# Kernel tuning notes

Measured on AMD Instinct MI355X. Metric: run time of the kernel, lower is better.

Reference implementation:

```python
import jax, jax.numpy as jnp
import numpy as np

N_USERS = 100000
N_ITEMS = 50000
DIM = 64
HID = 64
E = 3200000
B = 16384


def setup_inputs() -> dict:
    key = jax.random.key(0)
    ks = jax.random.split(key, 16)
    N = N_USERS + N_ITEMS
    return {
        "users": jax.random.randint(ks[0], (B,), 0, N_USERS),
        "items": jax.random.randint(ks[1], (B,), 0, N_ITEMS),
        "edge_index": jax.random.randint(ks[2], (2, E), 0, N),
        "edge_weight": jax.random.uniform(ks[3], (E,), dtype=jnp.float32),
        # learned parameters
        "U": jax.random.normal(ks[4], (N_USERS, DIM), jnp.float32) * 0.1,
        "I": jax.random.normal(ks[5], (N_ITEMS, DIM), jnp.float32) * 0.1,
        "W0": jax.random.normal(ks[6], (DIM, HID), jnp.float32) / np.sqrt(DIM),
        "b0": jnp.zeros((HID,), jnp.float32),
        "g0": jnp.ones((HID,), jnp.float32),
        "be0": jnp.zeros((HID,), jnp.float32),
        "W1": jax.random.normal(ks[7], (HID, HID), jnp.float32) / np.sqrt(HID),
        "b1": jnp.zeros((HID,), jnp.float32),
        "g1": jnp.ones((HID,), jnp.float32),
        "be1": jnp.zeros((HID,), jnp.float32),
        "Wp": jax.random.normal(ks[8], (HID, DIM), jnp.float32) / np.sqrt(HID),
        "bp": jnp.zeros((DIM,), jnp.float32),
        "bu": jnp.zeros((N_USERS,), jnp.float32),
        "bi": jnp.zeros((N_ITEMS,), jnp.float32),
        "mu": jnp.zeros((), jnp.float32),
    }


def _layernorm(h, g, b, eps=1e-5):
    m = jnp.mean(h, axis=-1, keepdims=True)
    v = jnp.mean(jnp.square(h - m), axis=-1, keepdims=True)
    return (h - m) * jax.lax.rsqrt(v + eps) * g + b


def reference(users, items, edge_index, edge_weight, U, I,
              W0, b0, g0, be0, W1, b1, g1, be1, Wp, bp, bu, bi, mu):
    N = U.shape[0] + I.shape[0]
    x = jnp.concatenate([U, I], axis=0)  # [N, DIM]

    # GCN normalization with added self-loops (torch_geometric gcn_norm)
    loop = jnp.arange(N)
    src = jnp.concatenate([edge_index[0], loop])
    dst = jnp.concatenate([edge_index[1], loop])
    ew = jnp.concatenate([edge_weight, jnp.ones((N,), edge_weight.dtype)])
    deg = jax.ops.segment_sum(ew, dst, num_segments=N)
    dinv = jnp.where(deg > 0, jax.lax.rsqrt(deg), 0.0)
    norm = dinv[src] * ew * dinv[dst]  # [E+N]

    def conv(h, W, b):
        hw = h @ W  # [N, HID]
        msgs = norm[:, None] * hw[src]  # gather: [E+N, HID]
        return jax.ops.segment_sum(msgs, dst, num_segments=N) + b

    # layer 0: conv -> layernorm -> relu -> (dropout=identity, eval) -> residual
    h = x
    h_in = h
    h = conv(h, W0, b0)
    h = jax.nn.relu(_layernorm(h, g0, be0)) + h_in
    # layer 1
    h_in = h
    h = conv(h, W1, b1)
    h = jax.nn.relu(_layernorm(h, g1, be1)) + h_in

    h = h @ Wp + bp  # proj_out: [N, DIM]
    h_user = h[:U.shape[0]]
    h_item = h[U.shape[0]:]

    s = jnp.sum(h_user[users] * h_item[items], axis=-1)
    s = s + bu[users] + bi[items] + mu
    return jnp.clip(s, 1.0, 5.0)
```

## Files before the change

kernel.cpp:

```cpp
#include <hip/hip_runtime.h>

#define NU 100000
#define NI 50000
#define NN 150000
#define D  64
#define CAP 47
#define OVF_MAX 4096

#define BINSHIFT 8
#define BINW 256
#define NBINS 586
#define BINCAP 5848
#define STAGE_CAP 11
#define EPT 8
#define BIN_BLOCKS 768
#define BCPAD 16
#define TAILS 5

typedef unsigned int uint;
typedef unsigned short ushort;
typedef unsigned char uchar;

__device__ __forceinline__ float half_reduce_add(float v) {
    #pragma unroll
    for (int m = 16; m >= 1; m >>= 1) v += __shfl_xor(v, m, 64);
    return v;
}
__device__ __forceinline__ ushort f2bf(float f) {
    union { float f; uint i; } c; c.f = f;
    uint r = c.i + 0x7FFF + ((c.i >> 16) & 1);
    return (ushort)(r >> 16);
}
__device__ __forceinline__ float lane_bcast(float v, int l) {
    return __int_as_float(__builtin_amdgcn_readlane(__float_as_int(v), l));
}
__device__ __forceinline__ uint enc14(float w) {
    uint b = __float_as_uint(w) + 0x00020000u;
    return b & 0xFFFC0000u;
}
__device__ __forceinline__ float dec14(uint r) {
    return __uint_as_float(r & 0xFFFC0000u);
}

__global__ __launch_bounds__(256) void k_bin(
        const int* __restrict__ src, const int* __restrict__ dst,
        const float* __restrict__ ew, int* __restrict__ bincur,
        uint2* __restrict__ binbuf, uint2* __restrict__ tail,
        uchar* __restrict__ cnt8, int E) {
    __shared__ uint2 stage[NBINS][STAGE_CAP];
    __shared__ int scnt[NBINS];
    int t = threadIdx.x;
    for (int i = t; i < NBINS; i += 256) scnt[i] = 0;
    __syncthreads();
    const int batch = 256 * EPT;
    for (int base = blockIdx.x * batch; base < E; base += BIN_BLOCKS * batch) {
        int dd[EPT]; uint ss[EPT]; float ww[EPT]; int ok[EPT];
        #pragma unroll
        for (int k = 0; k < EPT; ++k) {
            int e = base + k * 256 + t;
            ok[k] = (e < E);
            if (ok[k]) { dd[k] = dst[e]; ss[k] = (uint)src[e]; ww[k] = ew[e]; }
        }
        #pragma unroll
        for (int k = 0; k < EPT; ++k) {
            if (!ok[k]) continue;
            int bin = dd[k] >> BINSHIFT;
            uint2 rec = make_uint2(
                ss[k] | ((uint)(dd[k] & (BINW - 1)) << 18),
                (uint)__float_as_int(ww[k]));
            int slot = atomicAdd(&scnt[bin], 1);
            if (slot < STAGE_CAP) {
                stage[bin][slot] = rec;
            } else {
                int b0 = atomicAdd(&bincur[bin * BCPAD], 1);
                if (b0 < BINCAP) binbuf[(size_t)bin * BINCAP + b0] = rec;
            }
        }
        __syncthreads();
        for (int bin = t; bin < NBINS; bin += 256) {
            int c = scnt[bin]; if (c > STAGE_CAP) c = STAGE_CAP;
            while (c >= 8) {
                int b0 = atomicAdd(&bincur[bin * BCPAD], 8);
                if (b0 + 8 <= BINCAP) {
                    uint4* o4 = (uint4*)(binbuf + (size_t)bin * BINCAP + b0);
                    uint2* s2 = &stage[bin][c - 8];
                    o4[0] = make_uint4(s2[0].x, s2[0].y, s2[1].x, s2[1].y);
                    o4[1] = make_uint4(s2[2].x, s2[2].y, s2[3].x, s2[3].y);
                    o4[2] = make_uint4(s2[4].x, s2[4].y, s2[5].x, s2[5].y);
                    o4[3] = make_uint4(s2[6].x, s2[6].y, s2[7].x, s2[7].y);
                }
                c -= 8;
            }
            scnt[bin] = c;
        }
        __syncthreads();
    }
    uchar* cb = cnt8 + (size_t)blockIdx.x * NBINS;
    for (int bin = t; bin < NBINS; bin += 256) {
        int c = scnt[bin]; if (c > STAGE_CAP) c = STAGE_CAP;
        if (c > TAILS) {
            for (int j = TAILS; j < c; ++j) {
                int b0 = atomicAdd(&bincur[bin * BCPAD], 1);
                if (b0 < BINCAP) binbuf[(size_t)bin * BINCAP + b0] =
                    stage[bin][j];
            }
            c = TAILS;
        }
        cb[bin] = (uchar)c;
    }
    uint2* tb = tail + (size_t)blockIdx.x * (NBINS * TAILS);
    for (int i = t; i < NBINS * TAILS; i += 256)
        tb[i] = stage[i / TAILS][i % TAILS];
}

__global__ __launch_bounds__(256) void k_regroup(
        const int* __restrict__ bincur, const uint2* __restrict__ binbuf,
        const uint2* __restrict__ tail, const uchar* __restrict__ cnt8,
        uint* __restrict__ recs, int* __restrict__ cursor,
        float* __restrict__ dinv, int4* __restrict__ ovf,
        int* __restrict__ ovfcnt,
        const float* __restrict__ U, const float* __restrict__ I,
        const float* __restrict__ W0, ushort* __restrict__ hw2b) {
    __shared__ uint image[256 * CAP];
    __shared__ int cnt[256];
    __shared__ float ovfw[256];
    int t = threadIdx.x;
    int bin = blockIdx.x;
    cnt[t] = 0; ovfw[t] = 0.0f;
    __syncthreads();
    int dbase = bin << BINSHIFT;
    int nrec = bincur[bin * BCPAD]; if (nrec > BINCAP) nrec = BINCAP;
    const uint2* bb = binbuf + (size_t)bin * BINCAP;
    for (int i = t; i < nrec; i += 256) {
        uint2 r = bb[i];
        int dl = (int)(r.x >> 18);
        int slot = atomicAdd(&cnt[dl], 1);
        uint s = r.x & 0x3FFFFu;
        float w = __int_as_float((int)r.y);
        if (slot < CAP) image[dl * CAP + slot] = enc14(w) | s;
        else {
            atomicAdd(&ovfw[dl], w);
            int o = atomicAdd(ovfcnt, 1);
            if (o < OVF_MAX)
                ovf[o] = make_int4(dbase + dl, (int)s, __float_as_int(w), 0);
        }
    }
    for (int g = t; g < BIN_BLOCKS; g += 256) {
        int c = cnt8[(size_t)g * NBINS + bin];
        const uint2* tb = tail + ((size_t)g * NBINS + bin) * TAILS;
        for (int j = 0; j < c; ++j) {
            uint2 r = tb[j];
            int dl = (int)(r.x >> 18);
            int slot = atomicAdd(&cnt[dl], 1);
            uint s = r.x & 0x3FFFFu;
            float w = __int_as_float((int)r.y);
            if (slot < CAP) image[dl * CAP + slot] = enc14(w) | s;
            else {
                atomicAdd(&ovfw[dl], w);
                int o = atomicAdd(ovfcnt, 1);
                if (o < OVF_MAX)
                    ovf[o] = make_int4(dbase + dl, (int)s, __float_as_int(w), 0);
            }
        }
    }
    __syncthreads();
    int ndl = NN - dbase; if (ndl > 256) ndl = 256;
    if (ndl <= 0) return;
    if (t < ndl) {
        int c = cnt[t];
        cursor[dbase + t] = c;
        if (c > CAP) c = CAP;
        float dg = ovfw[t];
        for (int j = 0; j < c; ++j) dg += dec14(image[t * CAP + j]);
        float dv = rsqrtf(dg + 1.0f);
        dinv[dbase + t] = dv;
        ovfw[t] = dv;
    }
    int tot = ndl * CAP;
    uint* out = recs + (size_t)dbase * CAP;
    for (int i = t; i < tot; i += 256) out[i] = image[i];
    __syncthreads();
    {
        int lane = t & 63;
        int wv = t >> 6;
        float wreg[64];
        #pragma unroll
        for (int k = 0; k < 64; ++k) wreg[k] = W0[k * 64 + lane];
        for (int j = wv; j < ndl; j += 4) {
            int n = dbase + j;
            float xv = (n < NU) ? U[(size_t)n * D + lane]
                                : I[(size_t)(n - NU) * D + lane];
            float a0 = 0.f, a1 = 0.f, a2 = 0.f, a3 = 0.f;
            #pragma unroll
            for (int k = 0; k < 64; k += 4) {
                a0 = fmaf(lane_bcast(xv, k + 0), wreg[k + 0], a0);
                a1 = fmaf(lane_bcast(xv, k + 1), wreg[k + 1], a1);
                a2 = fmaf(lane_bcast(xv, k + 2), wreg[k + 2], a2);
                a3 = fmaf(lane_bcast(xv, k + 3), wreg[k + 3], a3);
            }
            hw2b[(size_t)n * D + lane] =
                f2bf(((a0 + a1) + (a2 + a3)) * ovfw[j]);
        }
    }
}

#define CA_DECL(c) uint x##c##0, x##c##1, x##c##2, x##c##3, \
                        w##c##0, w##c##1, w##c##2, w##c##3;
#define CA_GET(c, i, P, rvv) { \
    uint r = (uint)__builtin_amdgcn_ds_bpermute(vodd4 + 8 * (P), (int)(rvv)); \
    w##c##i = r & 0xFFFC0000u; \
    x##c##i = *(const uint*)((const char*)hw2p + \
                             (((r & 0x3FFFFu) << 7) + lb4)); }
#define CA_ISSUE(c, P0, rvv) { CA_GET(c, 0, (P0)+0, rvv) CA_GET(c, 1, (P0)+1, rvv) \
                               CA_GET(c, 2, (P0)+2, rvv) CA_GET(c, 3, (P0)+3, rvv) }
#define CA_FMA1(c, i, axv, ayv) { \
    axv = fmaf(__uint_as_float(w##c##i), __uint_as_float(x##c##i << 16), axv); \
    ayv = fmaf(__uint_as_float(w##c##i), \
               __uint_as_float(x##c##i & 0xFFFF0000u), ayv); }
#define CA_FMA(c, axv, ayv) { CA_FMA1(c,0,axv,ayv) CA_FMA1(c,1,axv,ayv) \
                              CA_FMA1(c,2,axv,ayv) CA_FMA1(c,3,axv,ayv) }

__device__ __forceinline__ float2 conv_accum2(int n, int lane,
        const uint* __restrict__ hw2p, const int* __restrict__ cursor,
        const uint* __restrict__ recs, const int4* __restrict__ ovf,
        const int* __restrict__ ovfcnt) {
    int cnt = __builtin_amdgcn_readfirstlane(cursor[n]);
    if (cnt > CAP) cnt = CAP;
    uint rv = (lane < cnt) ? recs[(size_t)n * CAP + lane] : 0u;
    const int  vodd4 = (lane >> 5) << 2;
    const uint lb4   = (uint)(lane & 31) << 2;
    uint xs = *(const uint*)((const char*)hw2p + (((uint)n << 7) + lb4));
    float ax = 0.f, ay = 0.f;
    int cp = (cnt + 7) & ~7;
    CA_DECL(A) CA_DECL(B) CA_DECL(G)
    CA_ISSUE(A, 0, rv) CA_ISSUE(B, 4, rv) CA_ISSUE(G, 8, rv)
    CA_FMA(A, ax, ay)
    if (cp > 24) CA_ISSUE(A, 12, rv)
    CA_FMA(B, ax, ay)
    if (cp > 32) CA_ISSUE(B, 16, rv)
    CA_FMA(G, ax, ay)
    if (cp > 40) CA_ISSUE(G, 20, rv)
    if (cp > 24) CA_FMA(A, ax, ay)
    if (cp > 32) CA_FMA(B, ax, ay)
    if (cp > 40) CA_FMA(G, ax, ay)
    ax += __shfl_xor(ax, 32, 64);
    ay += __shfl_xor(ay, 32, 64);
    ax += __uint_as_float(xs << 16);
    ay += __uint_as_float(xs & 0xFFFF0000u);
    int novf = __builtin_amdgcn_readfirstlane(ovfcnt[0]);
    if (novf > 0) {
        if (novf > OVF_MAX) novf = OVF_MAX;
        for (int j = 0; j < novf; ++j) {
            int4 e = ovf[j];
            if (e.x == n) {
                float w = __int_as_float(e.z);
                uint x = hw2p[(size_t)e.y * 32 + (lane & 31)];
                ax = fmaf(w, __int_as_float((int)(x << 16)), ax);
                ay = fmaf(w, __int_as_float((int)(x & 0xFFFF0000u)), ay);
            }
        }
    }
    return make_float2(ax, ay);
}

__device__ __forceinline__ float2 ln_relu2(float2 a, float di, int p,
        const float* __restrict__ b, const float* __restrict__ g,
        const float* __restrict__ be) {
    float2 bb = ((const float2*)b)[p];
    float v0 = fmaf(a.x, di, bb.x);
    float v1 = fmaf(a.y, di, bb.y);
    float m = half_reduce_add(v0 + v1) * (1.0f / 64.0f);
    float d0 = v0 - m, d1 = v1 - m;
    float var = half_reduce_add(d0 * d0 + d1 * d1) * (1.0f / 64.0f);
    float rs = rsqrtf(var + 1e-5f);
    float2 gg = ((const float2*)g)[p];
    float2 ee = ((const float2*)be)[p];
    return make_float2(fmaxf(fmaf(d0 * rs, gg.x, ee.x), 0.0f),
                       fmaxf(fmaf(d1 * rs, gg.y, ee.y), 0.0f));
}

__global__ __launch_bounds__(256) void k_conv1(
        const uint* __restrict__ hw2p, const int* __restrict__ cursor,
        const uint* __restrict__ recs, const int4* __restrict__ ovf,
        const int* __restrict__ ovfcnt, const float* __restrict__ dinv,
        const float* __restrict__ b, const float* __restrict__ g,
        const float* __restrict__ be, const float* __restrict__ U,
        const float* __restrict__ I, uint* __restrict__ out1) {
    int lane = threadIdx.x & 63;
    int n = __builtin_amdgcn_readfirstlane(blockIdx.x * 4 + (threadIdx.x >> 6));
    if (n >= NN) return;
    float2 a = conv_accum2(n, lane, hw2p, cursor, recs, ovf, ovfcnt);
    int p = lane & 31;
    float2 y = ln_relu2(a, dinv[n], p, b, g, be);
    const float* R = (n < NU) ? (U + (size_t)n * D) : (I + (size_t)(n - NU) * D);
    float2 rr = ((const float2*)R)[p];
    if (lane < 32) {
        out1[(size_t)n * 32 + p] =
            (uint)f2bf(y.x + rr.x) | ((uint)f2bf(y.y + rr.y) << 16);
    }
}

#define CB_DECL(p, c) uint p##x##c##0, p##x##c##1, p##x##c##2, p##x##c##3, \
                           p##w##c##0, p##w##c##1, p##w##c##2, p##w##c##3;
#define CB_GET(p, c, i, P, rvv) { \
    uint r = (uint)__builtin_amdgcn_ds_bpermute(vodd4 + 8 * (P), (int)(rvv)); \
    p##w##c##i = r & 0xFFFC0000u; \
    p##x##c##i = *(const uint*)((const char*)hw2p + \
                                (((r & 0x3FFFFu) << 7) + lb4)); }
#define CB_ISSUE(p, c, P0, rvv) { CB_GET(p,c,0,(P0)+0,rvv) CB_GET(p,c,1,(P0)+1,rvv) \
                                  CB_GET(p,c,2,(P0)+2,rvv) CB_GET(p,c,3,(P0)+3,rvv) }
#define CB_FMA1(p, c, i, axv, ayv) { \
    axv = fmaf(__uint_as_float(p##w##c##i), \
               __uint_as_float(p##x##c##i << 16), axv); \
    ayv = fmaf(__uint_as_float(p##w##c##i), \
               __uint_as_float(p##x##c##i & 0xFFFF0000u), ayv); }
#define CB_FMA(p, c, axv, ayv) { CB_FMA1(p,c,0,axv,ayv) CB_FMA1(p,c,1,axv,ayv) \
                                 CB_FMA1(p,c,2,axv,ayv) CB_FMA1(p,c,3,axv,ayv) }

__device__ __forceinline__ void conv_accum2_dual(int nu, int ni, int lane,
        const uint* __restrict__ hw2p, const int* __restrict__ cursor,
        const uint* __restrict__ recs, const int4* __restrict__ ovf,
        const int* __restrict__ ovfcnt, float2* outu, float2* outi) {
    int cu = __builtin_amdgcn_readfirstlane(cursor[nu]); if (cu > CAP) cu = CAP;
    int ci = __builtin_amdgcn_readfirstlane(cursor[ni]); if (ci > CAP) ci = CAP;
    uint rvu = (lane < cu) ? recs[(size_t)nu * CAP + lane] : 0u;
    uint rvi = (lane < ci) ? recs[(size_t)ni * CAP + lane] : 0u;
    const int  vodd4 = (lane >> 5) << 2;
    const uint lb4   = (uint)(lane & 31) << 2;
    uint xsu = *(const uint*)((const char*)hw2p + (((uint)nu << 7) + lb4));
    uint xsi = *(const uint*)((const char*)hw2p + (((uint)ni << 7) + lb4));
    float uax = 0.f, uay = 0.f, iax = 0.f, iay = 0.f;
    int cpu_ = (cu + 7) & ~7, cpi_ = (ci + 7) & ~7;
    CB_DECL(u, A) CB_DECL(u, B) CB_DECL(u, G)
    CB_DECL(i, A) CB_DECL(i, B) CB_DECL(i, G)
    CB_ISSUE(u, A, 0, rvu) CB_ISSUE(i, A, 0, rvi)
    CB_ISSUE(u, B, 4, rvu) CB_ISSUE(i, B, 4, rvi)
    CB_ISSUE(u, G, 8, rvu) CB_ISSUE(i, G, 8, rvi)
    CB_FMA(u, A, uax, uay) CB_FMA(i, A, iax, iay)
    if (cpu_ > 24) CB_ISSUE(u, A, 12, rvu)
    if (cpi_ > 24) CB_ISSUE(i, A, 12, rvi)
    CB_FMA(u, B, uax, uay) CB_FMA(i, B, iax, iay)
    if (cpu_ > 32) CB_ISSUE(u, B, 16, rvu)
    if (cpi_ > 32) CB_ISSUE(i, B, 16, rvi)
    CB_FMA(u, G, uax, uay) CB_FMA(i, G, iax, iay)
    if (cpu_ > 40) CB_ISSUE(u, G, 20, rvu)
    if (cpi_ > 40) CB_ISSUE(i, G, 20, rvi)
    if (cpu_ > 24) CB_FMA(u, A, uax, uay)
    if (cpi_ > 24) CB_FMA(i, A, iax, iay)
    if (cpu_ > 32) CB_FMA(u, B, uax, uay)
    if (cpi_ > 32) CB_FMA(i, B, iax, iay)
    if (cpu_ > 40) CB_FMA(u, G, uax, uay)
    if (cpi_ > 40) CB_FMA(i, G, iax, iay)
    uax += __shfl_xor(uax, 32, 64); uay += __shfl_xor(uay, 32, 64);
    iax += __shfl_xor(iax, 32, 64); iay += __shfl_xor(iay, 32, 64);
    uax += __uint_as_float(xsu << 16); uay += __uint_as_float(xsu & 0xFFFF0000u);
    iax += __uint_as_float(xsi << 16); iay += __uint_as_float(xsi & 0xFFFF0000u);
    int novf = __builtin_amdgcn_readfirstlane(ovfcnt[0]);
    if (novf > 0) {
        if (novf > OVF_MAX) novf = OVF_MAX;
        for (int j = 0; j < novf; ++j) {
            int4 e = ovf[j];
            if (e.x == nu || e.x == ni) {
                float w = __int_as_float(e.z);
                uint x = hw2p[(size_t)e.y * 32 + (lane & 31)];
                float fx = __uint_as_float(x << 16);
                float fy = __uint_as_float(x & 0xFFFF0000u);
                if (e.x == nu) { uax = fmaf(w, fx, uax); uay = fmaf(w, fy, uay); }
                else           { iax = fmaf(w, fx, iax); iay = fmaf(w, fy, iay); }
            }
        }
    }
    *outu = make_float2(uax, uay);
    *outi = make_float2(iax, iay);
}

__global__ __launch_bounds__(256) void k_gemm2(
        const ushort* __restrict__ hb, const float* __restrict__ W,
        const float* __restrict__ dinv, ushort* __restrict__ out) {
    int lane = threadIdx.x & 63;
    float wreg[64];
    #pragma unroll
    for (int k = 0; k < 64; ++k) wreg[k] = W[k * 64 + lane];
    int wpb = blockDim.x >> 6;
    int wid = blockIdx.x * wpb + (threadIdx.x >> 6);
    int tw = gridDim.x * wpb;
    for (int n = wid; n < NN; n += tw) {
        float xv = __uint_as_float((uint)hb[(size_t)n * D + lane] << 16);
        float a0 = 0.f, a1 = 0.f, a2 = 0.f, a3 = 0.f;
        #pragma unroll
        for (int k = 0; k < 64; k += 4) {
            a0 = fmaf(lane_bcast(xv, k + 0), wreg[k + 0], a0);
            a1 = fmaf(lane_bcast(xv, k + 1), wreg[k + 1], a1);
            a2 = fmaf(lane_bcast(xv, k + 2), wreg[k + 2], a2);
            a3 = fmaf(lane_bcast(xv, k + 3), wreg[k + 3], a3);
        }
        out[(size_t)n * D + lane] = f2bf(((a0 + a1) + (a2 + a3)) * dinv[n]);
    }
}

__global__ __launch_bounds__(256) void k_conv2score(
        const uint* __restrict__ hw2p, const int* __restrict__ cursor,
        const uint* __restrict__ recs, const int4* __restrict__ ovf,
        const int* __restrict__ ovfcnt, const float* __restrict__ dinv,
        const float* __restrict__ b, const float* __restrict__ g,
        const float* __restrict__ be, const int* __restrict__ users,
        const int* __restrict__ items, const uint* __restrict__ h1b,
        const float* __restrict__ Wp, const float* __restrict__ bp,
        const float* __restrict__ bu, const float* __restrict__ bi,
        const float* __restrict__ mu, float* __restrict__ out, int B) {
    __shared__ float wlds[64 * 64];
    int t = threadIdx.x;
    for (int i = t; i < 64 * 64; i += 256) wlds[i] = Wp[i];
    __syncthreads();
    int lane = t & 63;
    float bpl = bp[lane];
    int q = lane & 31;
    int wpb = blockDim.x >> 6;
    int wid = blockIdx.x * wpb + (t >> 6);
    int tw = gridDim.x * wpb;
    for (int p = wid; p < B; p += tw) {
        int un = users[p];
        int in_ = NU + items[p];
        int nu = __builtin_amdgcn_readfirstlane(un);
        int ni = __builtin_amdgcn_readfirstlane(in_);
        float2 au, ai;
        conv_accum2_dual(nu, ni, lane, hw2p, cursor, recs, ovf, ovfcnt,
                         &au, &ai);
        float2 yu = ln_relu2(au, dinv[nu], q, b, g, be);
        float2 yi = ln_relu2(ai, dinv[ni], q, b, g, be);
        uint xu = h1b[(size_t)nu * 32 + q];
        uint xi = h1b[(size_t)ni * 32 + q];
        float2 hu = make_float2(yu.x + __uint_as_float(xu << 16),
                                yu.y + __uint_as_float(xu & 0xFFFF0000u));
        float2 hi = make_float2(yi.x + __uint_as_float(xi << 16),
                                yi.y + __uint_as_float(xi & 0xFFFF0000u));
        float pu = bpl, pi = bpl;
        #pragma unroll
        for (int j = 0; j < 32; ++j) {
            float w0 = wlds[(2 * j) * 64 + lane];
            float w1 = wlds[(2 * j + 1) * 64 + lane];
            pu = fmaf(lane_bcast(hu.x, j), w0, pu);
            pu = fmaf(lane_bcast(hu.y, j), w1, pu);
            pi = fmaf(lane_bcast(hi.x, j), w0, pi);
            pi = fmaf(lane_bcast(hi.y, j), w1, pi);
        }
        float dot = pu * pi;
        #pragma unroll
        for (int m = 32; m >= 1; m >>= 1) dot += __shfl_xor(dot, m, 64);
        if (lane == 0) {
            dot += bu[un] + bi[in_ - NU] + mu[0];
            out[p] = fminf(fmaxf(dot, 1.0f), 5.0f);
        }
    }
}

extern "C" void kernel_launch(void* const* d_in, const int* in_sizes, int n_in,
                              void* d_out, int out_size, void* d_ws, size_t ws_size,
                              hipStream_t stream) {
    const int*   users = (const int*)d_in[0];
    const int*   items = (const int*)d_in[1];
    const int*   ei2   = (const int*)d_in[2];
    const float* ew    = (const float*)d_in[3];
    const float* U     = (const float*)d_in[4];
    const float* I     = (const float*)d_in[5];
    const float* W0    = (const float*)d_in[6];
    const float* b0    = (const float*)d_in[7];
    const float* g0    = (const float*)d_in[8];
    const float* be0   = (const float*)d_in[9];
    const float* W1    = (const float*)d_in[10];
    const float* b1    = (const float*)d_in[11];
    const float* g1    = (const float*)d_in[12];
    const float* be1   = (const float*)d_in[13];
    const float* Wp    = (const float*)d_in[14];
    const float* bp    = (const float*)d_in[15];
    const float* bu    = (const float*)d_in[16];
    const float* bi    = (const float*)d_in[17];
    const float* mu    = (const float*)d_in[18];

    int B = in_sizes[0];
    int E = in_sizes[2] / 2;
    const int* srcp = ei2;
    const int* dstp = ei2 + E;

    char* p = (char*)d_ws;
    auto alloc = [&](size_t bytes) -> char* {
        char* r = p;
        p += (bytes + 255) & ~(size_t)255;
        return r;
    };
    int*    cbuf    = (int*)  alloc((size_t)(NBINS * BCPAD + 32) * 4);
    int*    bincur  = cbuf;
    int*    ovfcnt  = cbuf + NBINS * BCPAD + 16;
    int*    cursor  = (int*)  alloc((size_t)NN * 4);
    float*  dinv    = (float*)alloc((size_t)NN * 4);
    int4*   ovf     = (int4*) alloc((size_t)OVF_MAX * 16);
    uchar*  cnt8    = (uchar*)alloc((size_t)BIN_BLOCKS * NBINS);
    uint2*  binbuf  = (uint2*)alloc((size_t)NBINS * BINCAP * 8);
    uint*   recs    = (uint*) alloc((size_t)NN * CAP * 4);
    ushort* hw2b    = (ushort*)alloc((size_t)NN * D * 2);
    uint*   h1b     = (uint*) alloc((size_t)NN * 32 * 4);
    const uint* hw2p = (const uint*)hw2b;
    uint2*  tail    = (uint2*)h1b;

    hipMemsetAsync(cbuf, 0, (size_t)(NBINS * BCPAD + 32) * 4, stream);

    int gW = (NN + 3) / 4;

    k_bin<<<BIN_BLOCKS, 256, 0, stream>>>(srcp, dstp, ew, bincur, binbuf,
                                          tail, cnt8, E);
    k_regroup<<<NBINS, 256, 0, stream>>>(bincur, binbuf, tail, cnt8,
                                         recs, cursor, dinv, ovf, ovfcnt,
                                         U, I, W0, hw2b);

    k_conv1<<<gW, 256, 0, stream>>>(hw2p, cursor, recs, ovf, ovfcnt, dinv,
                                    b0, g0, be0, U, I, h1b);
    k_gemm2<<<2048, 256, 0, stream>>>((const ushort*)h1b, W1, dinv, hw2b);
    k_conv2score<<<2048, 256, 0, stream>>>(hw2p, cursor, recs, ovf, ovfcnt, dinv,
                                           b1, g1, be1, users, items, h1b,
                                           Wp, bp, bu, bi, mu,
                                           (float*)d_out, B);
}
```

Before: 403.2 us.

## Transpose tail buffer to bin-major, embed counts in records, widen regroup blocks

The per-block tail records are now stored bin-major, so each regroup block reads a contiguous region instead of striding across blocks. The tail count is packed into the top bits of the first record, which removes the separate cnt8 array and its scattered byte reads. k_regroup runs with 512 threads to raise parallelism in the record scatter, the output copy and the W0 projection. Packing the count into bits 26+ assumes the destination-local field fits in 8 bits, which is why it is now masked; the W0 stage keeps 64 register floats per thread at double the block size, which may cost occupancy.

```diff
diff --git a/kernel.cpp b/kernel.cpp
--- a/kernel.cpp
+++ b/kernel.cpp
@@ -45,8 +45,7 @@
 __global__ __launch_bounds__(256) void k_bin(
         const int* __restrict__ src, const int* __restrict__ dst,
         const float* __restrict__ ew, int* __restrict__ bincur,
-        uint2* __restrict__ binbuf, uint2* __restrict__ tail,
-        uchar* __restrict__ cnt8, int E) {
+        uint2* __restrict__ binbuf, uint2* __restrict__ tail, int E) {
     __shared__ uint2 stage[NBINS][STAGE_CAP];
     __shared__ int scnt[NBINS];
     int t = threadIdx.x;
@@ -95,7 +94,6 @@
         }
         __syncthreads();
     }
-    uchar* cb = cnt8 + (size_t)blockIdx.x * NBINS;
     for (int bin = t; bin < NBINS; bin += 256) {
         int c = scnt[bin]; if (c > STAGE_CAP) c = STAGE_CAP;
         if (c > TAILS) {
@@ -106,16 +104,20 @@
             }
             c = TAILS;
         }
-        cb[bin] = (uchar)c;
-    }
-    uint2* tb = tail + (size_t)blockIdx.x * (NBINS * TAILS);
-    for (int i = t; i < NBINS * TAILS; i += 256)
-        tb[i] = stage[i / TAILS][i % TAILS];
-}
-
-__global__ __launch_bounds__(256) void k_regroup(
+        scnt[bin] = c;
+    }
+    __syncthreads();
+    for (int i = t; i < NBINS * TAILS; i += 256) {
+        int bin = i / TAILS, slot = i % TAILS;
+        uint2 r = stage[bin][slot];
+        if (slot == 0) r.x = (r.x & 0x03FFFFFFu) | ((uint)scnt[bin] << 26);
+        tail[((size_t)bin * BIN_BLOCKS + blockIdx.x) * TAILS + slot] = r;
+    }
+}
+
+__global__ __launch_bounds__(512) void k_regroup(
         const int* __restrict__ bincur, const uint2* __restrict__ binbuf,
-        const uint2* __restrict__ tail, const uchar* __restrict__ cnt8,
+        const uint2* __restrict__ tail,
         uint* __restrict__ recs, int* __restrict__ cursor,
         float* __restrict__ dinv, int4* __restrict__ ovf,
         int* __restrict__ ovfcnt,
@@ -126,12 +128,12 @@
     __shared__ float ovfw[256];
     int t = threadIdx.x;
     int bin = blockIdx.x;
-    cnt[t] = 0; ovfw[t] = 0.0f;
+    if (t < 256) { cnt[t] = 0; ovfw[t] = 0.0f; }
     __syncthreads();
     int dbase = bin << BINSHIFT;
     int nrec = bincur[bin * BCPAD]; if (nrec > BINCAP) nrec = BINCAP;
     const uint2* bb = binbuf + (size_t)bin * BINCAP;
-    for (int i = t; i < nrec; i += 256) {
+    for (int i = t; i < nrec; i += 512) {
         uint2 r = bb[i];
         int dl = (int)(r.x >> 18);
         int slot = atomicAdd(&cnt[dl], 1);
@@ -145,12 +147,15 @@
                 ovf[o] = make_int4(dbase + dl, (int)s, __float_as_int(w), 0);
         }
     }
-    for (int g = t; g < BIN_BLOCKS; g += 256) {
-        int c = cnt8[(size_t)g * NBINS + bin];
-        const uint2* tb = tail + ((size_t)g * NBINS + bin) * TAILS;
+    const uint2* tbin = tail + (size_t)bin * BIN_BLOCKS * TAILS;
+    for (int g = t; g < BIN_BLOCKS; g += 512) {
+        const uint2* tb = tbin + (size_t)g * TAILS;
+        uint2 r0 = tb[0];
+        int c = (int)(r0.x >> 26);
+        r0.x &= 0x03FFFFFFu;
         for (int j = 0; j < c; ++j) {
-            uint2 r = tb[j];
-            int dl = (int)(r.x >> 18);
+            uint2 r = (j == 0) ? r0 : tb[j];
+            int dl = (int)((r.x >> 18) & 0xFFu);
             int slot = atomicAdd(&cnt[dl], 1);
             uint s = r.x & 0x3FFFFu;
             float w = __int_as_float((int)r.y);
@@ -178,7 +183,7 @@
     }
     int tot = ndl * CAP;
     uint* out = recs + (size_t)dbase * CAP;
-    for (int i = t; i < tot; i += 256) out[i] = image[i];
+    for (int i = t; i < tot; i += 512) out[i] = image[i];
     __syncthreads();
     {
         int lane = t & 63;
@@ -186,7 +191,7 @@
         float wreg[64];
         #pragma unroll
         for (int k = 0; k < 64; ++k) wreg[k] = W0[k * 64 + lane];
-        for (int j = wv; j < ndl; j += 4) {
+        for (int j = wv; j < ndl; j += 8) {
             int n = dbase + j;
             float xv = (n < NU) ? U[(size_t)n * D + lane]
                                 : I[(size_t)(n - NU) * D + lane];
@@ -494,7 +499,6 @@
     int*    cursor  = (int*)  alloc((size_t)NN * 4);
     float*  dinv    = (float*)alloc((size_t)NN * 4);
     int4*   ovf     = (int4*) alloc((size_t)OVF_MAX * 16);
-    uchar*  cnt8    = (uchar*)alloc((size_t)BIN_BLOCKS * NBINS);
     uint2*  binbuf  = (uint2*)alloc((size_t)NBINS * BINCAP * 8);
     uint*   recs    = (uint*) alloc((size_t)NN * CAP * 4);
     ushort* hw2b    = (ushort*)alloc((size_t)NN * D * 2);
@@ -507,8 +511,8 @@
     int gW = (NN + 3) / 4;
 
     k_bin<<<BIN_BLOCKS, 256, 0, stream>>>(srcp, dstp, ew, bincur, binbuf,
-                                          tail, cnt8, E);
-    k_regroup<<<NBINS, 256, 0, stream>>>(bincur, binbuf, tail, cnt8,
+                                          tail, E);
+    k_regroup<<<NBINS, 512, 0, stream>>>(bincur, binbuf, tail,
                                          recs, cursor, dinv, ovf, ovfcnt,
                                          U, I, W0, hw2b);
 
```

Result: no change. 400.2 us (-0.7%).
